# Kernel tuning notes

Measured on AMD Instinct MI355X. Metric: run time of the kernel, lower is better.

## Reference

```python
import jax, jax.numpy as jnp
import numpy as np

BN_EPS = 1e-5
GRID = 8  # 8x8 region grid
AU_NUM = 12


def conv2d(x, w, b, stride=1, pad=0):
    # x: [B,C,H,W], w: [O,I,kh,kw]
    y = jax.lax.conv_general_dilated(
        x, w, (stride, stride), [(pad, pad), (pad, pad)],
        dimension_numbers=("NCHW", "OIHW", "NCHW"))
    return y + b[None, :, None, None]


def bn_eval(x, gamma, beta, mean, var):
    inv = jax.lax.rsqrt(var + BN_EPS)
    return (x - mean[None, :, None, None]) * (gamma * inv)[None, :, None, None] + beta[None, :, None, None]


def region_layer(x, gamma, beta, mean, var, cw, cb):
    # x: [B,C,H,W]; per-network params indexed by k = i*j + j (faithful to source)
    B, C, H, W = x.shape
    ph, pw = H // GRID, W // GRID
    # -> [64, B, C, ph, pw]
    p = x.reshape(B, C, GRID, ph, GRID, pw).transpose(2, 4, 0, 1, 3, 5).reshape(GRID * GRID, B, C, ph, pw)
    ii = jnp.arange(GRID)[:, None]
    jj = jnp.arange(GRID)[None, :]
    idx = (ii * jj + jj).reshape(-1)  # replicates self.networks[i*j+j]

    def per_patch(xp, g, bt, m, v, w, b):
        xn = bn_eval(xp, g, bt, m, v)
        xr = jax.nn.relu(xn)
        return conv2d(xr, w, b, stride=1, pad=1) + xp

    out = jax.vmap(per_patch)(p, gamma[idx], beta[idx], mean[idx], var[idx], cw[idx], cb[idx])
    # [64,B,C,ph,pw] -> [B,C,H,W]
    return out.reshape(GRID, GRID, B, C, ph, pw).transpose(2, 3, 0, 4, 1, 5).reshape(B, C, H, W)


def maxpool2(x):
    return jax.lax.reduce_window(x, -jnp.inf, jax.lax.max, (1, 1, 2, 2), (1, 1, 2, 2), "VALID")


def setup_inputs() -> dict:
    key = jax.random.key(0)
    ks = iter(jax.random.split(key, 40))
    n = lambda shape, s=0.05: jax.random.normal(next(ks), shape, jnp.float32) * s
    d = {}
    d["x"] = jax.random.normal(next(ks), (32, 3, 170, 170), jnp.float32)
    d["conv1_w"] = n((32, 3, 11, 11)); d["conv1_b"] = n((32,))
    NG = GRID * GRID
    d["rl_gamma"] = 1.0 + n((NG, 32)); d["rl_beta"] = n((NG, 32))
    d["rl_mean"] = n((NG, 32)); d["rl_var"] = 0.5 + jax.random.uniform(next(ks), (NG, 32), jnp.float32)
    d["rl_cw"] = n((NG, 32, 32, 3, 3)); d["rl_cb"] = n((NG, 32))
    d["bn_gamma"] = 1.0 + n((32,)); d["bn_beta"] = n((32,))
    d["bn_mean"] = n((32,)); d["bn_var"] = 0.5 + jax.random.uniform(next(ks), (32,), jnp.float32)
    d["conv2_w"] = n((16, 32, 8, 8)); d["conv2_b"] = n((16,))
    d["conv3_w"] = n((16, 16, 8, 8)); d["conv3_b"] = n((16,))
    d["conv4_w"] = n((16, 16, 6, 6)); d["conv4_b"] = n((16,))
    d["conv5_w"] = n((16, 16, 5, 5)); d["conv5_b"] = n((16,))
    d["fc1_w"] = n((4096, 16 * 27 * 27), 0.01); d["fc1_b"] = n((4096,))
    d["fc2_w"] = n((2048, 4096), 0.01); d["fc2_b"] = n((2048,))
    d["fc3_w"] = n((AU_NUM * 2, 2048), 0.01); d["fc3_b"] = n((AU_NUM * 2,))
    return d


def reference(x, conv1_w, conv1_b, rl_gamma, rl_beta, rl_mean, rl_var, rl_cw, rl_cb,
              bn_gamma, bn_beta, bn_mean, bn_var, conv2_w, conv2_b, conv3_w, conv3_b,
              conv4_w, conv4_b, conv5_w, conv5_b, fc1_w, fc1_b, fc2_w, fc2_b, fc3_w, fc3_b):
    B = x.shape[0]
    h = conv2d(x, conv1_w, conv1_b)                       # [B,32,160,160]
    h = region_layer(h, rl_gamma, rl_beta, rl_mean, rl_var, rl_cw, rl_cb)
    h = jax.nn.relu(h)
    h = maxpool2(h)                                       # [B,32,80,80]
    h = bn_eval(h, bn_gamma, bn_beta, bn_mean, bn_var)
    h = jax.nn.relu(conv2d(h, conv2_w, conv2_b))          # [B,16,73,73]
    h = jax.nn.relu(conv2d(h, conv3_w, conv3_b))          # [B,16,66,66]
    h = jax.nn.relu(conv2d(h, conv4_w, conv4_b, stride=2))  # [B,16,31,31]
    h = jax.nn.relu(conv2d(h, conv5_w, conv5_b))          # [B,16,27,27]
    h = h.reshape(B, -1)
    h = jax.nn.relu(h @ fc1_w.T + fc1_b)
    h = jax.nn.relu(h @ fc2_w.T + fc2_b)  # dropout = identity (eval)
    h = h @ fc3_w.T + fc3_b
    h = h.reshape(B, 2, AU_NUM)
    return jax.nn.log_softmax(h, axis=1)
```

## Files before the change

### kernel.cpp

```cpp
#include <hip/hip_runtime.h>
#include <hip/hip_bf16.h>

typedef __hip_bfloat16 bf16;
typedef __attribute__((ext_vector_type(8))) short short8;
typedef __attribute__((ext_vector_type(4))) float f32x4;
typedef __attribute__((ext_vector_type(16))) float f32x16;

__device__ __forceinline__ float b2f(const bf16 v){ return __bfloat162float(v); }
__device__ __forceinline__ float ld(const float* p, long i){ return p[i]; }
__device__ __forceinline__ float ld(const bf16*  p, long i){ return b2f(p[i]); }

__device__ __forceinline__ unsigned f2bf_u(float f){
    union { float f; unsigned u; } a; a.f = f;
    unsigned r = a.u + 0x7FFFu + ((a.u >> 16) & 1u);
    return r >> 16;
}

__device__ __forceinline__ short8 pack8(const float* v){
    union { __hip_bfloat162 h[4]; short8 s; } r;
    #pragma unroll
    for (int i=0;i<4;i++)
        r.h[i] = __float22bfloat162_rn(float2{v[2*i], v[2*i+1]});
    return r.s;
}

#define GLD_LDS16(g, l) __builtin_amdgcn_global_load_lds( \
    (const __attribute__((address_space(1))) void*)(g), \
    (__attribute__((address_space(3))) void*)(l), 16, 0, 0)

#define OFF_C1W   0
#define OFF_C1B   11616
#define OFF_RLG   11648
#define OFF_RLB   13696
#define OFF_RLM   15744
#define OFF_RLV   17792
#define OFF_RLCW  19840
#define OFF_RLCB  609664
#define OFF_BNG   611712
#define OFF_BNB   611744
#define OFF_BNM   611776
#define OFF_BNV   611808
#define OFF_C2W   611840
#define OFF_C2B   644608
#define OFF_C3W   644624
#define OFF_C3B   661008
#define OFF_C4W   661024
#define OFF_C4B   670240
#define OFF_C5W   670256
#define OFF_C5B   676656
#define OFF_F1B   676672
#define OFF_F2B   680768
#define OFF_F3B   682816
#define P_TOTAL   682840
#define OFF_WB2   P_TOTAL
#define OFF_WB3   (P_TOTAL + 16384)
#define OFF_WC1   (P_TOTAL + 16384 + 8192)
#define P_END     (OFF_WC1 + 8448)

#define SZ_RL  589824
#define SZ_WB2 32768
#define SZ_WB3 16384
#define SZ_WC1 16896

__global__ void k_sniff(const void* __restrict__ x, int* __restrict__ flag)
{
    const bf16* xb = (const bf16*)x;
    const float v = fabsf(b2f(xb[2*threadIdx.x]));
    const int ok = (v >= 1e-6f && v <= 1e6f) ? 1 : 0;
    __shared__ int cnt;
    if (threadIdx.x == 0) cnt = 0;
    __syncthreads();
    atomicAdd(&cnt, ok);
    __syncthreads();
    if (threadIdx.x == 0) *flag = (cnt >= 192) ? 0 : 1;
}

struct CvtArgs { const void* src[23]; int off[23]; const void* cw; const void* w2; const void* w3; int total; };

__device__ __forceinline__ float getv(const void* p, long i, bool isf){
    return isf ? ((const float*)p)[i] : b2f(((const bf16*)p)[i]);
}

__global__ __launch_bounds__(256) void k_cvt(CvtArgs a, const int* __restrict__ flag,
                                             float* __restrict__ P)
{
    const bool isf = (*flag != 0);
    const int i1 = a.total;
    const int i2 = i1 + SZ_RL;
    const int i3 = i2 + SZ_WB2;
    const int i4 = i3 + SZ_WB3;
    const int i5 = i4 + SZ_WC1;
    for (int idx = blockIdx.x*256 + threadIdx.x; idx < i5; idx += gridDim.x*256){
        if (idx < i1){
            if (idx >= OFF_RLCW && idx < OFF_RLCB) continue;
            int k = 0;
            #pragma unroll
            for (int j = 1; j < 23; j++) if (idx >= a.off[j]) k = j;
            P[idx] = getv(a.src[k], idx - a.off[k], isf);
        } else if (idx < i2){
            const int d = idx - i1;
            const int net = d / 9216, dn = d % 9216;
            const int tap = dn >> 10, rem = dn & 1023;
            const int half = rem >> 9, lane = (rem >> 3) & 63, j = rem & 7;
            const int co = half*16 + (lane & 15);
            const int ci = ((lane >> 4) << 3) + j;
            const long sidx = (long)((net*32 + co)*32 + ci)*9 + tap;
            ((unsigned short*)(P + OFF_RLCW))[d] = (unsigned short)f2bf_u(getv(a.cw, sidx, isf));
        } else if (idx < i3){
            const int d = idx - i2;
            const int j = d & 7, lane = (d >> 3) & 63, tap = d >> 9;
            const int n = lane & 15, k = ((lane >> 4) << 3) + j;
            const int ci = k, ky = tap >> 3, kx = tap & 7;
            const long sidx = (long)((n*32 + ci)*8 + ky)*8 + kx;
            ((unsigned short*)(P + OFF_WB2))[d] = (unsigned short)f2bf_u(getv(a.w2, sidx, isf));
        } else if (idx < i4){
            const int d = idx - i3;
            const int j = d & 7, lane = (d >> 3) & 63, pair = d >> 9;
            const int n = lane & 15, k = ((lane >> 4) << 3) + j;
            const int tsel = k >> 4, ci = k & 15;
            const int ky = pair >> 2, kx = ((pair & 3) << 1) + tsel;
            const long sidx = (long)((n*16 + ci)*8 + ky)*8 + kx;
            ((unsigned short*)(P + OFF_WB3))[d] = (unsigned short)f2bf_u(getv(a.w3, sidx, isf));
        } else {
            const int d = idx - i4;
            const int ky = d / 1536, rem = d % 1536;
            const int ch = rem >> 9, rem2 = rem & 511;
            const int lane = rem2 >> 3, j = rem2 & 7;
            const int co = lane & 31, h5 = lane >> 5;
            const int kx = ch*4 + h5*2 + (j >> 2), ci = j & 3;
            float v = 0.f;
            if (ci < 3 && kx < 11)
                v = getv(a.src[0], (long)((co*3 + ci)*11 + ky)*11 + kx, isf);
            ((unsigned short*)(P + OFF_WC1))[d] = (unsigned short)f2bf_u(v);
        }
    }
}

__global__ __launch_bounds__(256,3) void k_conv1M(const void* __restrict__ x,
        const int* __restrict__ flag, const float* __restrict__ P, float* __restrict__ out)
{
    __shared__ unsigned short xs[18*44*4];
    __shared__ unsigned short wsm[SZ_WC1];
    const int t = threadIdx.x;
    const int y0 = blockIdx.x*8, x0 = blockIdx.y*32, b = blockIdx.z;
    { const uint4* src = (const uint4*)(P + OFF_WC1);
      uint4* dst = (uint4*)wsm;
      for (int e=t; e<2112; e+=256) dst[e] = src[e]; }
    const bool isf = (*flag) != 0;
    for (int e=t; e<792; e+=256){
        const int r = e/44, c = e%44;
        const long base = ((long)(b*3)*170 + (y0+r))*170 + min(x0+c, 169);
        float v0, v1, v2;
        if (isf){
            const float* xf = (const float*)x;
            v0 = xf[base]; v1 = xf[base+28900]; v2 = xf[base+57800];
        } else {
            const bf16* xf = (const bf16*)x;
            v0 = b2f(xf[base]); v1 = b2f(xf[base+28900]); v2 = b2f(xf[base+57800]);
        }
        uint2 u;
        u.x = f2bf_u(v0) | (f2bf_u(v1) << 16);
        u.y = f2bf_u(v2);
        *(uint2*)&xs[(r*44+c)*4] = u;
    }
    __syncthreads();
    const int wave = t>>6, lane = t&63;
    const int n = lane & 31, h5 = lane >> 5;
    const int r0 = wave*2;
    f32x16 acc0 = {0.f}, acc1 = {0.f};
    #pragma unroll
    for (int e=0;e<16;e++){ acc0[e]=0.f; acc1[e]=0.f; }
    #pragma unroll 1
    for (int ky=0; ky<11; ky++){
        #pragma unroll
        for (int ch=0; ch<3; ch++){
            const short8 aw = *(const short8*)&wsm[((ky*3+ch)*64 + lane)*8];
            const int kx0 = ch*4 + h5*2;
            const int a0 = ((r0+ky)*44 + n + kx0)*4;
            const int a1 = ((r0+1+ky)*44 + n + kx0)*4;
            union { uint2 u2[2]; short8 s; } ub0, ub1;
            ub0.u2[0] = *(const uint2*)&xs[a0];
            ub0.u2[1] = *(const uint2*)&xs[a0+4];
            ub1.u2[0] = *(const uint2*)&xs[a1];
            ub1.u2[1] = *(const uint2*)&xs[a1+4];
            acc0 = __builtin_amdgcn_mfma_f32_32x32x16_bf16(aw, ub0.s, acc0, 0,0,0);
            acc1 = __builtin_amdgcn_mfma_f32_32x32x16_bf16(aw, ub1.s, acc1, 0,0,0);
        }
    }
    float* opb = out + ((long)b*25600 + (long)(y0+r0)*160 + x0 + n)*32;
    #pragma unroll
    for (int g=0; g<4; g++){
        const int co0 = 8*g + 4*h5;
        const f32x4 bv = *(const f32x4*)&P[OFF_C1B + co0];
        f32x4 s0, s1;
        #pragma unroll
        for (int r=0;r<4;r++){ s0[r] = acc0[4*g+r] + bv[r]; s1[r] = acc1[4*g+r] + bv[r]; }
        *(f32x4*)(opb + co0) = s0;
        *(f32x4*)(opb + 160*32 + co0) = s1;
    }
}

__global__ __launch_bounds__(256,2) void k_regionM(const float* __restrict__ in,
        const float* __restrict__ P, float* __restrict__ pooled)
{
    __shared__ unsigned short s_in[484*32];
    __shared__ unsigned short wsm[9216];
    __shared__ float sc[32], sh[32];
    const int t = threadIdx.x;
    const int b = blockIdx.x & 31, kk = blockIdx.x >> 5;
    const int gi = kk >> 3, gj = kk & 7;
    const int net = gj*(gi+1);
    const long pbase = ((long)b*25600 + (long)(gi*20)*160 + gj*20)*32;
    if (t < 32){
        const float inv = rsqrtf(P[OFF_RLV+net*32+t]+1e-5f)*P[OFF_RLG+net*32+t];
        sc[t] = inv; sh[t] = P[OFF_RLB+net*32+t] - P[OFF_RLM+net*32+t]*inv;
    }
    { const uint4* src = (const uint4*)((const unsigned short*)(P+OFF_RLCW) + (size_t)net*9216);
      uint4* dst = (uint4*)wsm;
      for (int e=t; e<1152; e+=256) dst[e] = src[e]; }
    __syncthreads();
    for (int e=t; e<1936; e+=256){
        const int o = e & 3, p = e >> 2;
        const int pr = p/22, pc = p%22;
        short8 pk = {0,0,0,0,0,0,0,0};
        if (pr>0 && pr<21 && pc>0 && pc<21){
            const long a = pbase + ((long)(pr-1)*160 + (pc-1))*32 + o*8;
            float v[8];
            *(f32x4*)&v[0] = *(const f32x4*)&in[a];
            *(f32x4*)&v[4] = *(const f32x4*)&in[a+4];
            #pragma unroll
            for (int j=0;j<8;j++){
                const int ci = o*8 + j;
                v[j] = fmaxf(fmaf(v[j], sc[ci], sh[ci]), 0.f);
            }
            pk = pack8(v);
        }
        *(short8*)&s_in[p*32 + o*8] = pk;
    }
    __syncthreads();
    const int wave = t>>6, lane = t&63;
    const int q = lane>>4, n = lane&15;
    const int dr = n>>2, dc = n&3;
    const int nt = (wave==0) ? 7 : 6;
    int trs[7], tcs[7];
    #pragma unroll
    for (int i=0;i<7;i++){ const int tt = 4*i + wave; trs[i] = tt/5; tcs[i] = tt - 5*(tt/5); }
    f32x4 acc[7][2];
    {   float bias_v[2][4];
        #pragma unroll
        for (int h=0;h<2;h++)
            #pragma unroll
            for (int r=0;r<4;r++) bias_v[h][r] = P[OFF_RLCB + net*32 + h*16 + q*4 + r];
        #pragma unroll
        for (int i=0;i<7;i++)
            #pragma unroll
            for (int h=0;h<2;h++)
                acc[i][h] = (f32x4){bias_v[h][0], bias_v[h][1], bias_v[h][2], bias_v[h][3]};
    }
    #pragma unroll 1
    for (int tap=0; tap<9; tap++){
        const int ky = tap/3, kx = tap - 3*(tap/3);
        const short8 a0 = *(const short8*)&wsm[(tap*2+0)*512 + lane*8];
        const short8 a1 = *(const short8*)&wsm[(tap*2+1)*512 + lane*8];
        #pragma unroll
        for (int i=0;i<7;i++){
            if (i < nt){
                const int srow = trs[i]*4 + dr + ky, scol = tcs[i]*4 + dc + kx;
                const short8 bx = *(const short8*)&s_in[(srow*22 + scol)*32 + q*8];
                acc[i][0] = __builtin_amdgcn_mfma_f32_16x16x32_bf16(a0, bx, acc[i][0], 0,0,0);
                acc[i][1] = __builtin_amdgcn_mfma_f32_16x16x32_bf16(a1, bx, acc[i][1], 0,0,0);
            }
        }
    }
    float bnsc[2][4], bnsh[2][4];
    #pragma unroll
    for (int h=0;h<2;h++)
        #pragma unroll
        for (int r=0;r<4;r++){
            const int co = h*16 + q*4 + r;
            const float inv = rsqrtf(P[OFF_BNV+co]+1e-5f)*P[OFF_BNG+co];
            bnsc[h][r] = inv; bnsh[h][r] = P[OFF_BNB+co] - P[OFF_BNM+co]*inv;
        }
    const bool wr = ((n & 5) == 0);
    #pragma unroll
    for (int i=0;i<7;i++){
        if (i < nt){
            const int prow = trs[i]*4 + dr, pcol = tcs[i]*4 + dc;
            const long ra = pbase + ((long)prow*160 + pcol)*32;
            const long pa0 = ((long)b*6400 + (long)(gi*10 + trs[i]*2 + (dr>>1))*80
                              + gj*10 + tcs[i]*2 + (dc>>1))*32;
            #pragma unroll
            for (int h=0;h<2;h++){
                const f32x4 res = *(const f32x4*)&in[ra + h*16 + q*4];
                f32x4 pv;
                #pragma unroll
                for (int r=0;r<4;r++){
                    float v = acc[i][h][r] + res[r];
                    v = fmaxf(v, 0.f);
                    v = fmaxf(v, __shfl_xor(v, 1, 64));
                    v = fmaxf(v, __shfl_xor(v, 4, 64));
                    pv[r] = fmaf(v, bnsc[h][r], bnsh[h][r]);
                }
                if (wr) *(f32x4*)&pooled[pa0 + h*16 + q*4] = pv;
            }
        }
    }
}

template<int CIN, int HIN, int WIN, int HOUT, int WOUT, bool NHWC_OUT>
__global__ __launch_bounds__(256) void k_convM(const float* __restrict__ in,
        const unsigned short* __restrict__ WB, const float* __restrict__ bias,
        float* __restrict__ out)
{
    constexpr int PP = 23;
    constexpr bool C32 = (CIN == 32);
    __shared__ unsigned short xs[PP*PP*CIN];
    __shared__ unsigned short ws[C32 ? 16*64*8 : 32*64*8];
    const int t = threadIdx.x;
    const int col0 = blockIdx.x*16, row0 = blockIdx.y*16, b = blockIdx.z;
    for (int e = t; e < PP*PP*(CIN/8); e += 256){
        const int o = e % (CIN/8), pix = e / (CIN/8);
        int rr = row0 + pix/PP; if (rr > HIN-1) rr = HIN-1;
        int cc = col0 + pix%PP; if (cc > WIN-1) cc = WIN-1;
        const float* gp = &in[((long)b*HIN*WIN + (long)rr*WIN + cc)*CIN + o*8];
        float v[8];
        *(f32x4*)&v[0] = *(const f32x4*)gp;
        *(f32x4*)&v[4] = *(const f32x4*)(gp+4);
        *(short8*)&xs[pix*CIN + o*8] = pack8(v);
    }
    const int wave = t>>6, lane = t&63;
    const int quad = lane>>4, n16 = lane&15;
    const float bv = bias[n16];
    f32x4 acc[4];
    #pragma unroll
    for (int mt=0;mt<4;mt++) acc[mt] = (f32x4){bv,bv,bv,bv};
    if constexpr (C32){
        for (int ch=0; ch<4; ch++){
            __syncthreads();
            const unsigned* src = (const unsigned*)WB + ch*4096;
            for (int e=t; e<4096; e+=256) ((unsigned*)ws)[e] = src[e];
            __syncthreads();
            #pragma unroll 1
            for (int tap=0; tap<16; tap++){
                const int tg = ch*16+tap, ky = tg>>3, kx = tg&7;
                const short8 bw = *(const short8*)&ws[(tap*64+lane)*8];
                #pragma unroll
                for (int mt=0; mt<4; mt++){
                    const int pr = wave*4+mt+ky, pc = n16+kx;
                    const short8 av = *(const short8*)&xs[(pr*PP+pc)*32 + quad*8];
                    acc[mt] = __builtin_amdgcn_mfma_f32_16x16x32_bf16(av, bw, acc[mt], 0,0,0);
                }
            }
        }
    } else {
        for (int e=t; e<8192; e+=256) ((unsigned*)ws)[e] = ((const unsigned*)WB)[e];
        __syncthreads();
        #pragma unroll 1
        for (int pair=0; pair<32; pair++){
            const int ky = pair>>2, kx0 = (pair&3)*2;
            const short8 bw = *(const short8*)&ws[(pair*64+lane)*8];
            #pragma unroll
            for (int mt=0; mt<4; mt++){
                const int pr = wave*4+mt+ky, pc = n16 + kx0 + (quad>>1);
                const short8 av = *(const short8*)&xs[(pr*PP+pc)*16 + (quad&1)*8];
                acc[mt] = __builtin_amdgcn_mfma_f32_16x16x32_bf16(av, bw, acc[mt], 0,0,0);
            }
        }
    }
    #pragma unroll
    for (int mt=0; mt<4; mt++){
        const int orow = row0 + wave*4 + mt;
        if (orow >= HOUT) continue;
        const int ocol = col0 + quad*4;
        #pragma unroll
        for (int r=0;r<4;r++){
            if (ocol + r < WOUT){
                if constexpr (NHWC_OUT)
                    out[((long)b*HOUT*WOUT + (long)orow*WOUT + ocol + r)*16 + n16] = fmaxf(acc[mt][r], 0.f);
                else
                    out[((long)(b*16 + n16)*HOUT + orow)*WOUT + ocol + r] = fmaxf(acc[mt][r], 0.f);
            }
        }
    }
}

template<int CIN, int COUT, int KS, int STRIDE, int HIN, int WIN, int HOUT, int WOUT,
         int NG, int OW, bool BF16OUT, int ROWPAD>
__global__ __launch_bounds__(256,2) void k_convN(const float* __restrict__ in,
        const float* __restrict__ w, const float* __restrict__ bias, void* __restrict__ outv)
{
    __shared__ float wl[CIN*KS*KS];
    const int co = blockIdx.y, b = blockIdx.z;
    for (int j=threadIdx.x; j<CIN*KS*KS; j+=blockDim.x) wl[j] = w[co*CIN*KS*KS + j];
    __syncthreads();
    const int i = blockIdx.x*blockDim.x + threadIdx.x;
    if (i >= HOUT*NG) return;
    const int y = i / NG, x0 = (i % NG) * OW;
    float acc[OW];
    const float bv = bias[co];
    #pragma unroll
    for (int j=0;j<OW;j++) acc[j]=bv;
    constexpr int SPAN = STRIDE*(OW-1) + KS;
    for (int ci=0; ci<CIN; ci++){
        #pragma unroll
        for (int ky=0; ky<KS; ky++){
            const float* ip = in + ((long)(b*CIN+ci)*HIN + (STRIDE*y+ky))*WIN + STRIDE*x0;
            float v[SPAN];
            #pragma unroll
            for (int j=0;j<SPAN;j++) v[j]=ip[j];
            const float* wr = &wl[(ci*KS+ky)*KS];
            #pragma unroll
            for (int kx=0;kx<KS;kx++){
                const float wv = wr[kx];
                #pragma unroll
                for (int j=0;j<OW;j++) acc[j] = fmaf(v[STRIDE*j+kx], wv, acc[j]);
            }
        }
    }
    if constexpr (BF16OUT){
        unsigned short* op = (unsigned short*)outv + (long)b*ROWPAD + (co*HOUT + y)*WOUT + x0;
        #pragma unroll
        for (int j=0;j<OW;j++)
            if (x0 + j < WOUT) op[j] = (unsigned short)f2bf_u(fmaxf(acc[j], 0.f));
    } else {
        float* op = (float*)outv + ((long)(b*COUT+co)*HOUT + y)*WOUT + x0;
        #pragma unroll
        for (int j=0;j<OW;j++)
            if (x0 + j < WOUT) op[j] = fmaxf(acc[j], 0.f);
    }
}

__global__ void k_binit(float* __restrict__ y, const float* __restrict__ bias, int N)
{
    const int i = blockIdx.x*256 + threadIdx.x;
    if (i < 32*N) y[i] = bias[i % N];
}

__global__ void k_fc1prep(float* __restrict__ y, const float* __restrict__ bias,
                          unsigned short* __restrict__ xp)
{
    const int i = blockIdx.x*256 + threadIdx.x;
    if (i < 32*4096) y[i] = bias[i & 4095];
    if (i < 19968){
        const int r = i / 624;
        xp[(long)r*12288 + 11664 + (i - r*624)] = 0;
    }
}

__global__ __launch_bounds__(256) void k_xpack(const float* __restrict__ in,
        unsigned short* __restrict__ out, int rows, int Ksrc, int Kdst, int relu)
{
    const int per = Kdst >> 3;
    const int i = blockIdx.x*256 + threadIdx.x;
    if (i >= rows*per) return;
    const int row = i / per, k = (i - row*per)*8;
    float v[8];
    if (k + 8 <= Ksrc){
        *(f32x4*)&v[0] = *(const f32x4*)&in[(long)row*Ksrc + k];
        *(f32x4*)&v[4] = *(const f32x4*)&in[(long)row*Ksrc + k + 4];
    } else {
        #pragma unroll
        for (int j=0;j<8;j++) v[j] = (k + j < Ksrc) ? in[(long)row*Ksrc + k + j] : 0.f;
    }
    if (relu){
        #pragma unroll
        for (int j=0;j<8;j++) v[j] = fmaxf(v[j], 0.f);
    }
    *(short8*)&out[(long)row*Kdst + k] = pack8(v);
}

template<typename WT>
__device__ __forceinline__ void fcl_body(const unsigned short* __restrict__ x,
        const WT* __restrict__ w, float* __restrict__ y,
        int Kw, int Khat, int N, int Kc, int Nvalid, unsigned char* lbuf)
{
    constexpr bool WF = __is_same(WT, float);
    const int t = threadIdx.x;
    const int wave = t>>6, lane = t&63;
    const int quad = lane>>4, n16 = lane&15;
    const int og = wave>>1, bh = wave&1;
    const int bx = blockIdx.x;
    const int start = blockIdx.y*Kc;
    int steps = 0;
    {   const int rem = Kw - start;
        const int sa = Kc >> 7;
        if (rem > 0){ steps = (rem + 127) >> 7; if (steps > sa) steps = sa; }
    }
    f32x4 acc = {0.f,0.f,0.f,0.f};
    const unsigned short* xp = x + (long)(bh*16 + n16)*Khat;
    const int row = og*16 + n16;

    auto stage = [&](int s, int bsel){
        const int k0 = start + (s<<7);
        const bool swz = (k0 + 128 <= Kw);
        unsigned char* base = lbuf + bsel*16384;
        if constexpr (WF){
            const int r0 = wave*8;
            #pragma unroll
            for (int c=0;c<4;c++){
                const int rr = r0 + 2*c + (lane>>5);
                const int cs = swz ? ((lane&31) ^ (rr&7)) : (lane&31);
                long koff = (long)k0 + cs*4;
                const float* ga = w + (long)(bx*32 + rr)*Kw + koff;
                if (!swz && (koff + 4 > Kw)) ga = w + (long)(bx*32 + rr)*Kw;
                GLD_LDS16(ga, base + (r0 + 2*c)*512);
            }
        } else {
            const int r0 = wave*8;
            #pragma unroll
            for (int c=0;c<2;c++){
                const int rr = r0 + 4*c + (lane>>4);
                const int cs = swz ? ((lane&15) ^ (rr&7)) : (lane&15);
                long koff = (long)k0 + cs*8;
                const WT* ga = w + (long)(bx*32 + rr)*Kw + koff;
                if (!swz && (koff + 8 > Kw)) ga = w + (long)(bx*32 + rr)*Kw;
                GLD_LDS16(ga, base + (r0 + 4*c)*256);
            }
        }
    };
    auto consume = [&](int s, int bsel){
        const int k0 = start + (s<<7);
        const bool swz = (k0 + 128 <= Kw);
        const unsigned char* base = lbuf + bsel*16384;
        #pragma unroll
        for (int kk=0; kk<4; kk++){
            const int ka = k0 + kk*32 + quad*8;
            const short8 x8 = *(const short8*)&xp[ka];
            short8 bw;
            if constexpr (WF){
                const int c0 = kk*8 + quad*2;
                const int p0 = swz ? (c0 ^ (row&7)) : c0;
                const int p1 = swz ? ((c0+1) ^ (row&7)) : (c0+1);
                float wv[8];
                *(f32x4*)&wv[0] = *(const f32x4*)&base[row*512 + p0*16];
                *(f32x4*)&wv[4] = *(const f32x4*)&base[row*512 + p1*16];
                bw = pack8(wv);
            } else {
                const int c0 = kk*4 + quad;
                const int p0 = swz ? (c0 ^ (row&7)) : c0;
                bw = *(const short8*)&base[row*256 + p0*16];
            }
            acc = __builtin_amdgcn_mfma_f32_16x16x32_bf16(x8, bw, acc, 0,0,0);
        }
    };

    if (steps > 0){
        stage(0, 0);
        __syncthreads();
        for (int s=0; s<steps; s++){
            if (s+1 < steps) stage(s+1, (s+1)&1);
            consume(s, s&1);
            __syncthreads();
        }
    }
    const int o = bx*32 + og*16 + n16;
    if (o < Nvalid){
        #pragma unroll
        for (int r=0;r<4;r++)
            atomicAdd(&y[(long)(bh*16 + quad*4 + r)*N + o], acc[r]);
    }
}

__global__ __launch_bounds__(256) void k_fcL(const unsigned short* __restrict__ x,
        const void* __restrict__ w, const int* __restrict__ flag,
        float* __restrict__ y, int Kw, int Khat, int N, int Kc, int Nvalid)
{
    __shared__ unsigned char lbuf[2*16384];
    if (*flag) fcl_body<float>(x, (const float*)w, y, Kw, Khat, N, Kc, Nvalid, lbuf);
    else       fcl_body<bf16 >(x, (const bf16 *)w, y, Kw, Khat, N, Kc, Nvalid, lbuf);
}

template<typename WT>
__device__ __forceinline__ void fcm_loop(const unsigned short* __restrict__ xp,
        const WT* __restrict__ wp, int start, int end, int quad, f32x4& acc)
{
    const int nfull = (end - start) >> 5;
    const int end32 = start + (nfull << 5);
    const int qo = quad*8;

    short8 xA, xB, xC;
    short8 bwA, bwB, bwC;
    f32x4 wA0, wA1, wB0, wB1, wC0, wC1;

    auto loadA = [&](int k0){
        const int ka = k0 + qo;
        xA = *(const short8*)&xp[ka];
        if constexpr (__is_same(WT, bf16)) bwA = *(const short8*)&wp[ka];
        else { wA0 = *(const f32x4*)&wp[ka]; wA1 = *(const f32x4*)&wp[ka+4]; }
    };
    auto loadB = [&](int k0){
        const int ka = k0 + qo;
        xB = *(const short8*)&xp[ka];
        if constexpr (__is_same(WT, bf16)) bwB = *(const short8*)&wp[ka];
        else { wB0 = *(const f32x4*)&wp[ka]; wB1 = *(const f32x4*)&wp[ka+4]; }
    };
    auto loadC = [&](int k0){
        const int ka = k0 + qo;
        xC = *(const short8*)&xp[ka];
        if constexpr (__is_same(WT, bf16)) bwC = *(const short8*)&wp[ka];
        else { wC0 = *(const f32x4*)&wp[ka]; wC1 = *(const f32x4*)&wp[ka+4]; }
    };
    auto compA = [&](){
        short8 bw;
        if constexpr (__is_same(WT, bf16)) bw = bwA;
        else { float wv[8]; *(f32x4*)&wv[0]=wA0; *(f32x4*)&wv[4]=wA1; bw = pack8(wv); }
        acc = __builtin_amdgcn_mfma_f32_16x16x32_bf16(xA, bw, acc, 0,0,0);
    };
    auto compB = [&](){
        short8 bw;
        if constexpr (__is_same(WT, bf16)) bw = bwB;
        else { float wv[8]; *(f32x4*)&wv[0]=wB0; *(f32x4*)&wv[4]=wB1; bw = pack8(wv); }
        acc = __builtin_amdgcn_mfma_f32_16x16x32_bf16(xB, bw, acc, 0,0,0);
    };
    auto compC = [&](){
        short8 bw;
        if constexpr (__is_same(WT, bf16)) bw = bwC;
        else { float wv[8]; *(f32x4*)&wv[0]=wC0; *(f32x4*)&wv[4]=wC1; bw = pack8(wv); }
        acc = __builtin_amdgcn_mfma_f32_16x16x32_bf16(xC, bw, acc, 0,0,0);
    };

    if (nfull >= 3){
        loadA(start); loadB(start+32); loadC(start+64);
        int j = 0;
        for (; j + 6 <= nfull; j += 3){
            compA(); loadA(start + ((j+3)<<5));
            compB(); loadB(start + ((j+4)<<5));
            compC(); loadC(start + ((j+5)<<5));
        }
        const int rem = nfull - j;
        if (rem == 3){ compA(); compB(); compC(); }
        else if (rem == 4){
            compA(); loadA(start + ((j+3)<<5));
            compB(); compC(); compA();
        } else {
            compA(); loadA(start + ((j+3)<<5));
            compB(); loadB(start + ((j+4)<<5));
            compC(); compA(); compB();
        }
    } else if (nfull == 2){
        loadA(start); loadB(start+32); compA(); compB();
    } else if (nfull == 1){
        loadA(start); compA();
    }
    if (end32 < end){
        const int ka = end32 + qo;
        float xv[8], wv[8];
        #pragma unroll
        for (int j=0;j<8;j++){
            const bool v = (ka + j) < end;
            xv[j] = v ? b2f(((const bf16*)xp)[ka+j]) : 0.f;
            wv[j] = v ? (float)ld(wp, ka+j) : 0.f;
        }
        acc = __builtin_amdgcn_mfma_f32_16x16x32_bf16(pack8(xv), pack8(wv), acc, 0,0,0);
    }
}

__global__ __launch_bounds__(256,4) void k_fcM(const unsigned short* __restrict__ x,
        const void* __restrict__ w, const int* __restrict__ flag,
        float* __restrict__ y, int K, int N, int Kc, int Nvalid)
{
    const int t = threadIdx.x;
    const int wave = t>>6, lane = t&63;
    const int quad = lane>>4, n16 = lane&15;
    const int og = wave>>1, bh = wave&1;
    const int o = blockIdx.x*32 + og*16 + n16;
    const int orow = (o < Nvalid) ? o : (Nvalid-1);
    const int xrow = bh*16 + n16;
    const int start = blockIdx.y*Kc;
    const int end = min(K, start + Kc);
    f32x4 acc = {0.f,0.f,0.f,0.f};
    const unsigned short* xp = x + (long)xrow*K;
    if (*flag) fcm_loop<float>(xp, (const float*)w + (long)orow*K, start, end, quad, acc);
    else       fcm_loop<bf16 >(xp, (const bf16 *)w + (long)orow*K, start, end, quad, acc);
    if (o < Nvalid){
        #pragma unroll
        for (int r=0;r<4;r++)
            atomicAdd(&y[(long)(bh*16 + quad*4 + r)*N + o], acc[r]);
    }
}

__global__ void k_lsm(const float* __restrict__ in, const int* __restrict__ flag,
                      void* __restrict__ out)
{
    const int i = threadIdx.x;
    if (i >= 384) return;
    const int b = i/12, au = i%12;
    const float a0 = in[b*24+au], a1 = in[b*24+12+au];
    const float m = fmaxf(a0,a1);
    const float lse = m + logf(expf(a0-m)+expf(a1-m));
    const float o0 = a0-lse, o1 = a1-lse;
    if (*flag){
        ((float*)out)[b*24+au]    = o0;
        ((float*)out)[b*24+12+au] = o1;
    } else {
        ((bf16*)out)[b*24+au]    = __float2bfloat16(o0);
        ((bf16*)out)[b*24+12+au] = __float2bfloat16(o1);
    }
}

extern "C" void kernel_launch(void* const* d_in, const int* in_sizes, int n_in,
                              void* d_out, int out_size, void* d_ws, size_t ws_size,
                              hipStream_t stream) {
    (void)in_sizes; (void)n_in; (void)out_size; (void)ws_size;
    const void* x = d_in[0];

    float* A = (float*)d_ws;
    float* B = A + 26214400;
    float* P = B + 6553600;
    int* flag = (int*)(P + P_END);
    unsigned short* Xp = (unsigned short*)(P + P_END + 16);

    CvtArgs a;
    const int src_idx[23] = {1,2,3,4,5,6,7,8,9,10,11,12,13,14,15,16,17,18,19,20,22,24,26};
    const int offs[23] = {OFF_C1W,OFF_C1B,OFF_RLG,OFF_RLB,OFF_RLM,OFF_RLV,OFF_RLCW,OFF_RLCB,
                          OFF_BNG,OFF_BNB,OFF_BNM,OFF_BNV,OFF_C2W,OFF_C2B,OFF_C3W,OFF_C3B,
                          OFF_C4W,OFF_C4B,OFF_C5W,OFF_C5B,OFF_F1B,OFF_F2B,OFF_F3B};
    for (int j=0;j<23;j++){ a.src[j] = d_in[src_idx[j]]; a.off[j] = offs[j]; }
    a.cw = d_in[7]; a.w2 = d_in[13]; a.w3 = d_in[15];
    a.total = P_TOTAL;

    k_sniff<<<1,256,0,stream>>>(x, flag);
    k_cvt<<<(P_TOTAL+SZ_RL+SZ_WB2+SZ_WB3+SZ_WC1+255)/256,256,0,stream>>>(a, flag, P);
    k_conv1M<<<dim3(20,5,32),256,0,stream>>>(x, flag, P, A);
    k_regionM<<<2048,256,0,stream>>>(A, P, B);
    k_convM<32,80,80,73,73,true><<<dim3(5,5,32),256,0,stream>>>(B, (const unsigned short*)(P+OFF_WB2), P+OFF_C2B, A);
    k_convM<16,73,73,66,66,false><<<dim3(5,5,32),256,0,stream>>>(A, (const unsigned short*)(P+OFF_WB3), P+OFF_C3B, B);
    k_convN<16,16,6,2,66,66,31,31,8,4,false,0><<<dim3(1,16,32),256,0,stream>>>(B, P+OFF_C4W, P+OFF_C4B, A);
    k_convN<16,16,5,1,31,31,27,27,7,4,true,12288><<<dim3(1,16,32),256,0,stream>>>(A, P+OFF_C5W, P+OFF_C5B, Xp);
    k_fc1prep<<<512,256,0,stream>>>(A, P+OFF_F1B, Xp);
    k_fcL<<<dim3(128,16),256,0,stream>>>(Xp, d_in[21], flag, A, 11664, 12288, 4096, 768, 4096);
    k_xpack<<<(32*(4096/8)+255)/256,256,0,stream>>>(A, Xp, 32, 4096, 4096, 1);
    k_binit<<<(32*2048+255)/256,256,0,stream>>>(B, P+OFF_F2B, 2048);
    k_fcL<<<dim3(64,16),256,0,stream>>>(Xp, d_in[23], flag, B, 4096, 4096, 2048, 256, 2048);
    k_xpack<<<(32*(2048/8)+255)/256,256,0,stream>>>(B, Xp, 32, 2048, 2048, 1);
    k_binit<<<(32*24+255)/256,256,0,stream>>>(A, P+OFF_F3B, 24);
    k_fcM<<<dim3(1,64),256,0,stream>>>(Xp, d_in[25], flag, A, 2048, 24, 32, 24);
    k_lsm<<<1,384,0,stream>>>(A, flag, d_out);
}
```

Measured before the change: 586.6 us.

## Store conv1, region and conv2 intermediates in bf16 instead of fp32

Conv1 output, the region-layer pooled output and the conv2 output are now written as bf16 in global memory, and the consuming kernels read bf16 directly. The region kernel unpacks bf16 for its BN input and for the residual, and conv2/conv3 copy bf16 straight into LDS without repacking. This roughly halves the memory traffic of the large early activations (conv1 output alone is about 105 MB in fp32). The trade-off is extra rounding on the residual path and on intermediate activations, which could affect accuracy.

```diff
diff --git a/kernel.cpp b/kernel.cpp
--- a/kernel.cpp
+++ b/kernel.cpp
@@ -22,6 +22,27 @@
     for (int i=0;i<4;i++)
         r.h[i] = __float22bfloat162_rn(float2{v[2*i], v[2*i+1]});
     return r.s;
+}
+
+__device__ __forceinline__ uint2 pack4(const float* v){
+    union { __hip_bfloat162 h[2]; uint2 u; } r;
+    r.h[0] = __float22bfloat162_rn(float2{v[0], v[1]});
+    r.h[1] = __float22bfloat162_rn(float2{v[2], v[3]});
+    return r.u;
+}
+
+__device__ __forceinline__ void unp8(uint4 u, float* v){
+    union { unsigned x; float f; } a;
+    a.x = u.x<<16; v[0]=a.f; a.x = u.x&0xffff0000u; v[1]=a.f;
+    a.x = u.y<<16; v[2]=a.f; a.x = u.y&0xffff0000u; v[3]=a.f;
+    a.x = u.z<<16; v[4]=a.f; a.x = u.z&0xffff0000u; v[5]=a.f;
+    a.x = u.w<<16; v[6]=a.f; a.x = u.w&0xffff0000u; v[7]=a.f;
+}
+
+__device__ __forceinline__ void unp4(uint2 u, float* v){
+    union { unsigned x; float f; } a;
+    a.x = u.x<<16; v[0]=a.f; a.x = u.x&0xffff0000u; v[1]=a.f;
+    a.x = u.y<<16; v[2]=a.f; a.x = u.y&0xffff0000u; v[3]=a.f;
 }
 
 #define GLD_LDS16(g, l) __builtin_amdgcn_global_load_lds( \
@@ -137,7 +158,7 @@
 }
 
 __global__ __launch_bounds__(256,3) void k_conv1M(const void* __restrict__ x,
-        const int* __restrict__ flag, const float* __restrict__ P, float* __restrict__ out)
+        const int* __restrict__ flag, const float* __restrict__ P, unsigned short* __restrict__ out)
 {
     __shared__ unsigned short xs[18*44*4];
     __shared__ unsigned short wsm[SZ_WC1];
@@ -187,21 +208,21 @@
             acc1 = __builtin_amdgcn_mfma_f32_32x32x16_bf16(aw, ub1.s, acc1, 0,0,0);
         }
     }
-    float* opb = out + ((long)b*25600 + (long)(y0+r0)*160 + x0 + n)*32;
+    unsigned short* opb = out + ((long)b*25600 + (long)(y0+r0)*160 + x0 + n)*32;
     #pragma unroll
     for (int g=0; g<4; g++){
         const int co0 = 8*g + 4*h5;
         const f32x4 bv = *(const f32x4*)&P[OFF_C1B + co0];
-        f32x4 s0, s1;
+        float s0[4], s1[4];
         #pragma unroll
         for (int r=0;r<4;r++){ s0[r] = acc0[4*g+r] + bv[r]; s1[r] = acc1[4*g+r] + bv[r]; }
-        *(f32x4*)(opb + co0) = s0;
-        *(f32x4*)(opb + 160*32 + co0) = s1;
-    }
-}
-
-__global__ __launch_bounds__(256,2) void k_regionM(const float* __restrict__ in,
-        const float* __restrict__ P, float* __restrict__ pooled)
+        *(uint2*)(opb + co0) = pack4(s0);
+        *(uint2*)(opb + 160*32 + co0) = pack4(s1);
+    }
+}
+
+__global__ __launch_bounds__(256,2) void k_regionM(const unsigned short* __restrict__ in,
+        const float* __restrict__ P, unsigned short* __restrict__ pooled)
 {
     __shared__ unsigned short s_in[484*32];
     __shared__ unsigned short wsm[9216];
@@ -225,9 +246,9 @@
         short8 pk = {0,0,0,0,0,0,0,0};
         if (pr>0 && pr<21 && pc>0 && pc<21){
             const long a = pbase + ((long)(pr-1)*160 + (pc-1))*32 + o*8;
+            const uint4 u = *(const uint4*)&in[a];
             float v[8];
-            *(f32x4*)&v[0] = *(const f32x4*)&in[a];
-            *(f32x4*)&v[4] = *(const f32x4*)&in[a+4];
+            unp8(u, v);
             #pragma unroll
             for (int j=0;j<8;j++){
                 const int ci = o*8 + j;
@@ -291,8 +312,10 @@
                               + gj*10 + tcs[i]*2 + (dc>>1))*32;
             #pragma unroll
             for (int h=0;h<2;h++){
-                const f32x4 res = *(const f32x4*)&in[ra + h*16 + q*4];
-                f32x4 pv;
+                const uint2 ru = *(const uint2*)&in[ra + h*16 + q*4];
+                float res[4];
+                unp4(ru, res);
+                float pv[4];
                 #pragma unroll
                 for (int r=0;r<4;r++){
                     float v = acc[i][h][r] + res[r];
@@ -301,16 +324,16 @@
                     v = fmaxf(v, __shfl_xor(v, 4, 64));
                     pv[r] = fmaf(v, bnsc[h][r], bnsh[h][r]);
                 }
-                if (wr) *(f32x4*)&pooled[pa0 + h*16 + q*4] = pv;
+                if (wr) *(uint2*)&pooled[pa0 + h*16 + q*4] = pack4(pv);
             }
         }
     }
 }
 
 template<int CIN, int HIN, int WIN, int HOUT, int WOUT, bool NHWC_OUT>
-__global__ __launch_bounds__(256) void k_convM(const float* __restrict__ in,
+__global__ __launch_bounds__(256) void k_convM(const unsigned short* __restrict__ in,
         const unsigned short* __restrict__ WB, const float* __restrict__ bias,
-        float* __restrict__ out)
+        void* __restrict__ outv)
 {
     constexpr int PP = 23;
     constexpr bool C32 = (CIN == 32);
@@ -322,11 +345,8 @@
         const int o = e % (CIN/8), pix = e / (CIN/8);
         int rr = row0 + pix/PP; if (rr > HIN-1) rr = HIN-1;
         int cc = col0 + pix%PP; if (cc > WIN-1) cc = WIN-1;
-        const float* gp = &in[((long)b*HIN*WIN + (long)rr*WIN + cc)*CIN + o*8];
-        float v[8];
-        *(f32x4*)&v[0] = *(const f32x4*)gp;
-        *(f32x4*)&v[4] = *(const f32x4*)(gp+4);
-        *(short8*)&xs[pix*CIN + o*8] = pack8(v);
+        const uint4 v = *(const uint4*)&in[((long)b*HIN*WIN + (long)rr*WIN + cc)*CIN + o*8];
+        *(uint4*)&xs[pix*CIN + o*8] = v;
     }
     const int wave = t>>6, lane = t&63;
     const int quad = lane>>4, n16 = lane&15;
@@ -375,10 +395,12 @@
         #pragma unroll
         for (int r=0;r<4;r++){
             if (ocol + r < WOUT){
+                const float v = fmaxf(acc[mt][r], 0.f);
                 if constexpr (NHWC_OUT)
-                    out[((long)b*HOUT*WOUT + (long)orow*WOUT + ocol + r)*16 + n16] = fmaxf(acc[mt][r], 0.f);
+                    ((unsigned short*)outv)[((long)b*HOUT*WOUT + (long)orow*WOUT + ocol + r)*16 + n16]
+                        = (unsigned short)f2bf_u(v);
                 else
-                    out[((long)(b*16 + n16)*HOUT + orow)*WOUT + ocol + r] = fmaxf(acc[mt][r], 0.f);
+                    ((float*)outv)[((long)(b*16 + n16)*HOUT + orow)*WOUT + ocol + r] = v;
             }
         }
     }
@@ -709,6 +731,8 @@
     float* P = B + 6553600;
     int* flag = (int*)(P + P_END);
     unsigned short* Xp = (unsigned short*)(P + P_END + 16);
+    unsigned short* Abf = (unsigned short*)A;
+    unsigned short* Bbf = (unsigned short*)B;
 
     CvtArgs a;
     const int src_idx[23] = {1,2,3,4,5,6,7,8,9,10,11,12,13,14,15,16,17,18,19,20,22,24,26};
@@ -721,10 +745,10 @@
 
     k_sniff<<<1,256,0,stream>>>(x, flag);
     k_cvt<<<(P_TOTAL+SZ_RL+SZ_WB2+SZ_WB3+SZ_WC1+255)/256,256,0,stream>>>(a, flag, P);
-    k_conv1M<<<dim3(20,5,32),256,0,stream>>>(x, flag, P, A);
-    k_regionM<<<2048,256,0,stream>>>(A, P, B);
-    k_convM<32,80,80,73,73,true><<<dim3(5,5,32),256,0,stream>>>(B, (const unsigned short*)(P+OFF_WB2), P+OFF_C2B, A);
-    k_convM<16,73,73,66,66,false><<<dim3(5,5,32),256,0,stream>>>(A, (const unsigned short*)(P+OFF_WB3), P+OFF_C3B, B);
+    k_conv1M<<<dim3(20,5,32),256,0,stream>>>(x, flag, P, Abf);
+    k_regionM<<<2048,256,0,stream>>>(Abf, P, Bbf);
+    k_convM<32,80,80,73,73,true><<<dim3(5,5,32),256,0,stream>>>(Bbf, (const unsigned short*)(P+OFF_WB2), P+OFF_C2B, (void*)Abf);
+    k_convM<16,73,73,66,66,false><<<dim3(5,5,32),256,0,stream>>>(Abf, (const unsigned short*)(P+OFF_WB3), P+OFF_C3B, (void*)B);
     k_convN<16,16,6,2,66,66,31,31,8,4,false,0><<<dim3(1,16,32),256,0,stream>>>(B, P+OFF_C4W, P+OFF_C4B, A);
     k_convN<16,16,5,1,31,31,27,27,7,4,true,12288><<<dim3(1,16,32),256,0,stream>>>(A, P+OFF_C5W, P+OFF_C5B, Xp);
     k_fc1prep<<<512,256,0,stream>>>(A, P+OFF_F1B, Xp);
```

Result: no change. 584.0 us (-0.4%).
